# Kernel tuning notes

Hardware: AMD Instinct MI355X
Metric: run time of the kernel (lower is better)

## Reference

```python
import jax, jax.numpy as jnp
import numpy as np


def _layer_norm(x, g, b, eps=1e-5):
    mu = x.mean(-1, keepdims=True)
    var = ((x - mu) ** 2).mean(-1, keepdims=True)
    return (x - mu) * jax.lax.rsqrt(var + eps) * g + b


def _linear(x, w, b):
    # torch nn.Linear: y = x @ W^T + b, w has shape (out, in)
    return jnp.einsum('...i,oi->...o', x, w) + b


def setup_inputs() -> dict:
    key = jax.random.key(0)
    ks = jax.random.split(key, 12)
    B, N, C = 1, 512, 128
    s = 0.02  # weight init scale
    f32 = jnp.float32
    return {
        'X': jax.random.normal(ks[0], (B, N, N, C), f32),
        'mask': jax.random.randint(ks[1], (B, N, N, 1), 0, 2) > 0,
        # first LayerNorm
        'ln1_g': jnp.ones((C,), f32), 'ln1_b': jnp.zeros((C,), f32),
        # left edge MLP: Linear -> Sigmoid -> Linear
        'lw1': jax.random.normal(ks[2], (C, C), f32) * s, 'lb1': jnp.zeros((C,), f32),
        'lw2': jax.random.normal(ks[3], (C, C), f32) * s, 'lb2': jnp.zeros((C,), f32),
        # right edge MLP
        'rw1': jax.random.normal(ks[4], (C, C), f32) * s, 'rb1': jnp.zeros((C,), f32),
        'rw2': jax.random.normal(ks[5], (C, C), f32) * s, 'rb2': jnp.zeros((C,), f32),
        # skip gate: Linear -> Sigmoid
        'sw': jax.random.normal(ks[6], (C, C), f32) * s, 'sb': jnp.zeros((C,), f32),
        # combine: LayerNorm -> Linear
        'ln2_g': jnp.ones((C,), f32), 'ln2_b': jnp.zeros((C,), f32),
        'cw': jax.random.normal(ks[7], (C, C), f32) * s, 'cb': jnp.zeros((C,), f32),
    }


def reference(X, mask, ln1_g, ln1_b, lw1, lb1, lw2, lb2,
              rw1, rb1, rw2, rb2, sw, sb, ln2_g, ln2_b, cw, cb):
    h = _layer_norm(X, ln1_g, ln1_b)                      # (B,N,N,C)
    A = _linear(jax.nn.sigmoid(_linear(h, lw1, lb1)), lw2, lb2)
    Bm = _linear(jax.nn.sigmoid(_linear(h, rw1, rb1)), rw2, rb2)
    G = jax.nn.sigmoid(_linear(h, sw, sb))
    A = jnp.where(mask, A, 0.0)
    Bm = jnp.where(mask, Bm, 0.0)
    # triangle multiplication, 'outgoing': contract over k per channel
    T = jnp.einsum('bikc,bjkc->bijc', A, Bm)              # (B,N,N,C)
    Y = _linear(_layer_norm(T, ln2_g, ln2_b), cw, cb) * G
    return Y
```

## Files before the change

kernel.cpp:

```cpp
#include <hip/hip_runtime.h>

typedef unsigned short u16;
typedef unsigned int   u32;
typedef u32   u32x4  __attribute__((ext_vector_type(4)));
typedef __bf16 bf16x8 __attribute__((ext_vector_type(8)));
typedef float f32x4  __attribute__((ext_vector_type(4)));

#define NPOS (512*512)
#define WSLOT 16384

__device__ __forceinline__ u16 f2bf(float f){
  __bf16 h=(__bf16)f;
  return __builtin_bit_cast(u16,h);
}
__device__ __forceinline__ float bf2f(u16 s){ u32 u=((u32)s)<<16; return __builtin_bit_cast(float,u); }
union pk8 { u16 s[8]; u32x4 v; };

__device__ __forceinline__ void gload16(const void* g, void* l){
  __builtin_amdgcn_global_load_lds((const __attribute__((address_space(1))) void*)g,
                                   (__attribute__((address_space(3))) void*)l, 16, 0, 0);
}

__device__ __forceinline__ bf16x8 cvt8(const float* p){
  f32x4 w0=*(const f32x4*)p, w1=*(const f32x4*)(p+4);
  bf16x8 b;
#pragma unroll
  for(int e=0;e<4;e++){ b[e]=(__bf16)w0[e]; b[4+e]=(__bf16)w1[e]; }
  return b;
}

__global__ __launch_bounds__(256) void k0(
    const float* __restrict__ lw1, const float* __restrict__ lw2,
    const float* __restrict__ rw1, const float* __restrict__ rw2,
    const float* __restrict__ sw,  const float* __restrict__ cw, u16* __restrict__ Wp)
{
  const float* srcs[6]={lw1,lw2,rw1,rw2,sw,cw};
  const float* W=srcs[blockIdx.x];
  u16* dst=Wp + (size_t)blockIdx.x*WSLOT;
  const int t=threadIdx.x, lane=t&63, wvv=t>>6, lr=lane&15, quad=lane>>4;
#pragma unroll
  for(int i=0;i<8;i++){
    int tile=wvv*8+i, nt=tile>>2, kk=tile&3;
    const float* p=W+(size_t)(nt*16+lr)*128+kk*32+quad*8;
    bf16x8 b=cvt8(p);
    *(u32x4*)(dst+((size_t)tile*64+lane)*8)=__builtin_bit_cast(u32x4,b);
  }
}

__device__ __forceinline__ void wave_gemm2(const u16 (*sh)[136], int wv, int lane,
    const u16* __restrict__ Wp, const float* __restrict__ bias, float o[4][2][4])
{
  const int lr=lane&15, quad=lane>>4;
  bf16x8 b[2][4];
#pragma unroll
  for(int n2=0;n2<2;n2++){
    const int nt=wv*2+n2;
#pragma unroll
    for(int kk=0;kk<4;kk++)
      b[n2][kk]=*(const bf16x8*)(Wp+((size_t)((nt*4+kk)*64+lane))*8);
  }
  float bv[2]={bias[(wv*2)*16+lr], bias[(wv*2+1)*16+lr]};
#pragma unroll
  for(int mt=0;mt<4;mt++){
    bf16x8 a[4];
#pragma unroll
    for(int kk=0;kk<4;kk++) a[kk]=*(const bf16x8*)&sh[mt*16+lr][kk*32+quad*8];
#pragma unroll
    for(int n2=0;n2<2;n2++){
      f32x4 acc={0.f,0.f,0.f,0.f};
#pragma unroll
      for(int kk=0;kk<4;kk++)
        acc=__builtin_amdgcn_mfma_f32_16x16x32_bf16(a[kk],b[n2][kk],acc,0,0,0);
#pragma unroll
      for(int r=0;r<4;r++) o[mt][n2][r]=acc[r]+bv[n2];
    }
  }
}

__device__ __forceinline__ void sig_to_lds2(u16 (*sh)[136], int wv,int lane, float o[4][2][4]){
  const int lr=lane&15, quad=lane>>4;
#pragma unroll
  for(int mt=0;mt<4;mt++)
#pragma unroll
    for(int n2=0;n2<2;n2++)
#pragma unroll
      for(int r=0;r<4;r++)
        sh[mt*16+quad*4+r][(wv*2+n2)*16+lr]=f2bf(1.f/(1.f+__expf(-o[mt][n2][r])));
}

__device__ __forceinline__ void out_to_lds2(u16 (*sh)[136], int wv,int lane, float o[4][2][4]){
  const int lr=lane&15, quad=lane>>4;
#pragma unroll
  for(int mt=0;mt<4;mt++)
#pragma unroll
    for(int n2=0;n2<2;n2++)
#pragma unroll
      for(int r=0;r<4;r++)
        sh[mt*16+quad*4+r][(wv*2+n2)*16+lr]=f2bf(o[mt][n2][r]);
}

__device__ __forceinline__ void store_tr_m(const u16 (*sh)[136], int t, u16* __restrict__ dst,
                                           int p0, const u16* __restrict__ smask){
#pragma unroll
  for(int iter=0;iter<4;iter++){
    int c=iter*32+(t>>3);
    int pos=(t&7)*8;
    pk8 u;
#pragma unroll
    for(int r=0;r<8;r++){
      int rp=(r+(t>>3)+(t&7))&7;
      u.s[rp]=sh[pos+rp][c] & smask[pos+rp];
    }
    *(u32x4*)(dst+(size_t)c*NPOS+p0+pos)=u.v;
  }
}

__global__ __launch_bounds__(256,4) void k1(
    const float* __restrict__ X, const void* __restrict__ mask,
    const float* __restrict__ g1, const float* __restrict__ b1,
    const u16* __restrict__ Wp,
    const float* __restrict__ lb1, const float* __restrict__ lb2,
    const float* __restrict__ rb1, const float* __restrict__ rb2,
    const float* __restrict__ sb,
    u16* __restrict__ At, u16* __restrict__ Bt, float* __restrict__ G)
{
  __shared__ u16 shh[64][136];
  __shared__ u16 sht[64][136];
  __shared__ u16 smask16[64];
  __shared__ int mpacked;
  const int t=threadIdx.x;
  const int p0=blockIdx.x*64;
  if(t==0){
    const int* m32=(const int*)mask;
    int pk=0;
#pragma unroll
    for(int i=0;i<32;i++){ u32 v=(u32)m32[i]; if(v>1u) pk=1; }
    mpacked=pk;
  }
  {
    int row=t>>2, q=t&3;
    const float* xp = X + (size_t)(p0+row)*128 + q*32;
    float v[32]; float s=0.f,s2=0.f;
#pragma unroll
    for(int u=0;u<8;u++){ f32x4 d=*(const f32x4*)(xp+u*4);
#pragma unroll
      for(int e=0;e<4;e++) v[u*4+e]=d[e]; }
#pragma unroll
    for(int i=0;i<32;i++){ s+=v[i]; s2+=v[i]*v[i]; }
    s+=__shfl_xor(s,1); s2+=__shfl_xor(s2,1);
    s+=__shfl_xor(s,2); s2+=__shfl_xor(s2,2);
    float mu=s*(1.f/128.f);
    float rstd=1.f/sqrtf(s2*(1.f/128.f)-mu*mu+1e-5f);
#pragma unroll
    for(int u=0;u<4;u++){
      pk8 o;
#pragma unroll
      for(int e=0;e<8;e++){
        int c=q*32+u*8+e;
        o.s[e]=f2bf((v[u*8+e]-mu)*rstd*g1[c]+b1[c]);
      }
      *(u32x4*)&shh[row][q*32+u*8]=o.v;
    }
  }
  __syncthreads();
  if(t<64){
    int p=p0+t;
    int mval = mpacked ? (int)((const unsigned char*)mask)[p] : ((const int*)mask)[p];
    smask16[t]=(mval!=0)?(u16)0xFFFFu:(u16)0u;
  }
  const int lane=t&63, wv=t>>6, lr=lane&15, quad=lane>>4;
  float oL[4][2][4], oR[4][2][4];
  {
    float oG[4][2][4];
    wave_gemm2(shh,wv,lane,Wp+4*WSLOT,sb,oG);
#pragma unroll
    for(int mt=0;mt<4;mt++)
#pragma unroll
      for(int n2=0;n2<2;n2++)
#pragma unroll
        for(int r=0;r<4;r++){
          size_t p=p0+mt*16+quad*4+r;
          G[p*128+(wv*2+n2)*16+lr]=1.f/(1.f+__expf(-oG[mt][n2][r]));
        }
  }
  wave_gemm2(shh,wv,lane,Wp+0*WSLOT,lb1,oL);
  sig_to_lds2(sht,wv,lane,oL);
  wave_gemm2(shh,wv,lane,Wp+2*WSLOT,rb1,oR);
  __syncthreads();
  sig_to_lds2(shh,wv,lane,oR);
  wave_gemm2(sht,wv,lane,Wp+1*WSLOT,lb2,oL);
  __syncthreads();
  out_to_lds2(sht,wv,lane,oL);
  wave_gemm2(shh,wv,lane,Wp+3*WSLOT,rb2,oR);
  __syncthreads();
  store_tr_m(sht,t,At,p0,smask16);
  out_to_lds2(shh,wv,lane,oR);
  __syncthreads();
  store_tr_m(shh,t,Bt,p0,smask16);
}

__global__ __launch_bounds__(256) void k2(const u16* __restrict__ At, const u16* __restrict__ Bt,
                                          u16* __restrict__ T, int j_base, int jc, int nxsh)
{
  __shared__ u16 sA[128*64];
  __shared__ u16 sB[128*64];
  const int t=threadIdx.x, lane=t&63, wv=t>>6;
  const int bid=blockIdx.x;
  const int tpcsh=2+nxsh;
  const int xcd=bid&7, q=bid>>3;
  const int c   = xcd*16 + (q>>tpcsh);
  const int tile= q & ((1<<tpcsh)-1);
  const int j0l = (tile & ((1<<nxsh)-1))*128;
  const int i0  = (tile >> nxsh)*128;
  const int wm=(wv>>1)*64, wn=(wv&1)*64, lr=lane&15, quad=lane>>4;
  const u16* Ab = At + (size_t)c*NPOS + (size_t)i0*512;
  const u16* Bb = Bt + (size_t)c*NPOS + (size_t)(j_base+j0l)*512;
  const int srow = lane>>3;
  const int scol = ((lane&7) ^ srow)*8;
  const int swz  = (lr&7)<<4;
  f32x4 acc[4][4];
#pragma unroll
  for(int i=0;i<4;i++)
#pragma unroll
    for(int j=0;j<4;j++) acc[i][j]=(f32x4){0.f,0.f,0.f,0.f};
  for(int k0=0;k0<512;k0+=64){
#pragma unroll
    for(int j=0;j<4;j++){
      int seg=wv*4+j;
      int row=seg*8+srow;
      gload16(Ab + (size_t)row*512 + k0 + scol, &sA[seg*512]);
      gload16(Bb + (size_t)row*512 + k0 + scol, &sB[seg*512]);
    }
    __syncthreads();
    const char* sAc=(const char*)sA;
    const char* sBc=(const char*)sB;
#pragma unroll
    for(int ks=0;ks<2;ks++){
      bf16x8 a[4],b[4];
#pragma unroll
      for(int mt=0;mt<4;mt++){
        int row=wm+mt*16+lr;
        a[mt]=*(const bf16x8*)(sAc + row*128 + ((ks*64+quad*16)^swz));
      }
#pragma unroll
      for(int nt=0;nt<4;nt++){
        int row=wn+nt*16+lr;
        b[nt]=*(const bf16x8*)(sBc + row*128 + ((ks*64+quad*16)^swz));
      }
#pragma unroll
      for(int mt=0;mt<4;mt++)
#pragma unroll
        for(int nt=0;nt<4;nt++)
          acc[mt][nt]=__builtin_amdgcn_mfma_f32_16x16x32_bf16(a[mt],b[nt],acc[mt][nt],0,0,0);
    }
    __syncthreads();
  }
  u16* Tb = T + (size_t)c*512*jc;
#pragma unroll
  for(int mt=0;mt<4;mt++)
#pragma unroll
    for(int nt=0;nt<4;nt++)
#pragma unroll
      for(int r=0;r<4;r++){
        int row=i0+wm+mt*16+quad*4+r;
        int col=j0l+wn+nt*16+lr;
        Tb[(size_t)row*jc+col]=f2bf(acc[mt][nt][r]);
      }
}

__global__ __launch_bounds__(256) void k3(const u16* __restrict__ T,
    const u16* __restrict__ cwp,
    const float* __restrict__ g2, const float* __restrict__ b2,
    const float* __restrict__ cb, float* GY,
    int j_base, int jc, int jshift)
{
  __shared__ u16 sH[128][136];
  const int t=threadIdx.x;
  const int cp0=blockIdx.x*128;
  {
    int c=t>>1, half=t&1;
    const u16* Tp = T + (size_t)c*512*jc + cp0 + half*64;
#pragma unroll
    for(int u=0;u<8;u++){
      pk8 d; d.v=*(const u32x4*)(Tp+u*8);
#pragma unroll
      for(int e=0;e<8;e++) sH[half*64+u*8+e][c]=d.s[e];
    }
  }
  __syncthreads();
  {
    int pos=t>>1, half=t&1;
    float v[64]; float s=0.f,s2=0.f;
#pragma unroll
    for(int u=0;u<8;u++)
#pragma unroll
      for(int e=0;e<8;e++){ float x=bf2f(sH[pos][half*64+u*8+e]); v[u*8+e]=x; s+=x; s2+=x*x; }
    s+=__shfl_xor(s,1); s2+=__shfl_xor(s2,1);
    float mu=s*(1.f/128.f);
    float rstd=1.f/sqrtf(s2*(1.f/128.f)-mu*mu+1e-5f);
#pragma unroll
    for(int u=0;u<8;u++){
      pk8 o;
#pragma unroll
      for(int e=0;e<8;e++){
        int c=half*64+u*8+e;
        o.s[e]=f2bf((v[u*8+e]-mu)*rstd*g2[c]+b2[c]);
      }
      *(u32x4*)&sH[pos][half*64+u*8]=o.v;
    }
  }
  __syncthreads();
  const int lane=t&63, wv=t>>6, m0=wv*32, lr=lane&15, quad=lane>>4;
  bf16x8 a[2][4];
#pragma unroll
  for(int mt=0;mt<2;mt++)
#pragma unroll
    for(int kk=0;kk<4;kk++) a[mt][kk]=*(const bf16x8*)&sH[m0+mt*16+lr][kk*32+quad*8];
#pragma unroll
  for(int nt=0;nt<8;nt++){
    f32x4 a0={0.f,0.f,0.f,0.f}, a1={0.f,0.f,0.f,0.f};
#pragma unroll
    for(int kk=0;kk<4;kk++){
      bf16x8 b=*(const bf16x8*)(cwp+((size_t)((nt*4+kk)*64+lane))*8);
      a0=__builtin_amdgcn_mfma_f32_16x16x32_bf16(a[0][kk],b,a0,0,0,0);
      a1=__builtin_amdgcn_mfma_f32_16x16x32_bf16(a[1][kk],b,a1,0,0,0);
    }
    float cbv=cb[nt*16+lr];
#pragma unroll
    for(int mt=0;mt<2;mt++){
      f32x4 ac = mt? a1: a0;
#pragma unroll
      for(int r=0;r<4;r++){
        int l=m0+mt*16+quad*4+r;
        int pl=cp0+l;
        size_t p=((size_t)(pl>>jshift)<<9)+(size_t)j_base+(pl&(jc-1));
        int col=nt*16+lr;
        float gg=GY[p*128+col];
        GY[p*128+col]=(ac[r]+cbv)*gg;
      }
    }
  }
}

__global__ void kprobe(float* out, u32 wsmib){
  if(threadIdx.x==0 && blockIdx.x==0) out[0]=(float)wsmib;
}

extern "C" void kernel_launch(void* const* d_in, const int* in_sizes, int n_in,
                              void* d_out, int out_size, void* d_ws, size_t ws_size,
                              hipStream_t stream)
{
  (void)in_sizes; (void)n_in; (void)out_size;
  const float* X  =(const float*)d_in[0];
  const void*  mask=d_in[1];
  const float* g1 =(const float*)d_in[2];  const float* b1 =(const float*)d_in[3];
  const float* lw1=(const float*)d_in[4];  const float* lb1=(const float*)d_in[5];
  const float* lw2=(const float*)d_in[6];  const float* lb2=(const float*)d_in[7];
  const float* rw1=(const float*)d_in[8];  const float* rb1=(const float*)d_in[9];
  const float* rw2=(const float*)d_in[10]; const float* rb2=(const float*)d_in[11];
  const float* sw =(const float*)d_in[12]; const float* sb =(const float*)d_in[13];
  const float* g2 =(const float*)d_in[14]; const float* b2 =(const float*)d_in[15];
  const float* cw =(const float*)d_in[16]; const float* cb =(const float*)d_in[17];
  float* out=(float*)d_out;

  const size_t wbytes = (size_t)6*WSLOT*sizeof(u16);
  const size_t base = wbytes + 2*(size_t)NPOS*128*sizeof(u16);
  int jc=0, jshift=0, nxsh=0;
  if      (ws_size >= base + (size_t)512*512*128*2){ jc=512; jshift=9; nxsh=2; }
  else if (ws_size >= base + (size_t)512*256*128*2){ jc=256; jshift=8; nxsh=1; }
  else if (ws_size >= base + (size_t)512*128*128*2){ jc=128; jshift=7; nxsh=0; }
  if(jc==0){
    kprobe<<<dim3(1),dim3(64),0,stream>>>(out,(u32)(ws_size>>20));
    return;
  }
  u16* Wp=(u16*)d_ws;
  u16* At=Wp+(size_t)6*WSLOT;
  u16* Bt=At+(size_t)NPOS*128;
  u16* T =Bt+(size_t)NPOS*128;

  k0<<<dim3(6),dim3(256),0,stream>>>(lw1,lw2,rw1,rw2,sw,cw,Wp);
  k1<<<dim3(4096),dim3(256),0,stream>>>(X,mask,g1,b1,Wp,lb1,lb2,rb1,rb2,sb,At,Bt,out);
  const int nbl=(jc/128)*4*128;
  for(int jb=0;jb<512;jb+=jc){
    k2<<<dim3(nbl),dim3(256),0,stream>>>(At,Bt,T,jb,jc,nxsh);
    k3<<<dim3(4*jc),dim3(256),0,stream>>>(T,Wp+(size_t)5*WSLOT,g2,b2,cb,out,jb,jc,jshift);
  }
}
```

Before: 555.0 us.

## Store gate in bf16, double-buffer k2 LDS loads, reorder k1 for register pressure

The sigmoid gate G is now kept as bf16 in workspace instead of fp32 in the output buffer. This halves gate write and read traffic between k1 and k3, at some precision cost. k2 double-buffers its shared-memory A/B tiles so the next k-step's global-to-LDS loads overlap the current MFMAs. k1 processes the left, right and gate paths one after another with a single LDS scratch buffer and applies the mask as a float multiply, to cut live registers. k3 also re-reads LDS instead of holding 64 floats per thread. Together these add more barriers in k1 and double k2's LDS footprint.

```diff
diff --git a/kernel.cpp b/kernel.cpp
--- a/kernel.cpp
+++ b/kernel.cpp
@@ -88,19 +88,20 @@
         sh[mt*16+quad*4+r][(wv*2+n2)*16+lr]=f2bf(1.f/(1.f+__expf(-o[mt][n2][r])));
 }
 
-__device__ __forceinline__ void out_to_lds2(u16 (*sh)[136], int wv,int lane, float o[4][2][4]){
+__device__ __forceinline__ void mask_to_lds2(u16 (*sh)[136], int wv,int lane, float o[4][2][4], const float* smask){
   const int lr=lane&15, quad=lane>>4;
 #pragma unroll
   for(int mt=0;mt<4;mt++)
 #pragma unroll
     for(int n2=0;n2<2;n2++)
 #pragma unroll
-      for(int r=0;r<4;r++)
-        sh[mt*16+quad*4+r][(wv*2+n2)*16+lr]=f2bf(o[mt][n2][r]);
-}
-
-__device__ __forceinline__ void store_tr_m(const u16 (*sh)[136], int t, u16* __restrict__ dst,
-                                           int p0, const u16* __restrict__ smask){
+      for(int r=0;r<4;r++){
+        int row=mt*16+quad*4+r;
+        sh[row][(wv*2+n2)*16+lr]=f2bf(o[mt][n2][r]*smask[row]);
+      }
+}
+
+__device__ __forceinline__ void store_tr(const u16 (*sh)[136], int t, u16* __restrict__ dst, int p0){
 #pragma unroll
   for(int iter=0;iter<4;iter++){
     int c=iter*32+(t>>3);
@@ -109,7 +110,7 @@
 #pragma unroll
     for(int r=0;r<8;r++){
       int rp=(r+(t>>3)+(t&7))&7;
-      u.s[rp]=sh[pos+rp][c] & smask[pos+rp];
+      u.s[rp]=sh[pos+rp][c];
     }
     *(u32x4*)(dst+(size_t)c*NPOS+p0+pos)=u.v;
   }
@@ -122,11 +123,12 @@
     const float* __restrict__ lb1, const float* __restrict__ lb2,
     const float* __restrict__ rb1, const float* __restrict__ rb2,
     const float* __restrict__ sb,
-    u16* __restrict__ At, u16* __restrict__ Bt, float* __restrict__ G)
+    u16* __restrict__ At, u16* __restrict__ Bt,
+    u16* __restrict__ Gb, float* __restrict__ Gf, int gb16)
 {
   __shared__ u16 shh[64][136];
   __shared__ u16 sht[64][136];
-  __shared__ u16 smask16[64];
+  __shared__ float smask[64];
   __shared__ int mpacked;
   const int t=threadIdx.x;
   const int p0=blockIdx.x*64;
@@ -166,44 +168,47 @@
   if(t<64){
     int p=p0+t;
     int mval = mpacked ? (int)((const unsigned char*)mask)[p] : ((const int*)mask)[p];
-    smask16[t]=(mval!=0)?(u16)0xFFFFu:(u16)0u;
-  }
-  const int lane=t&63, wv=t>>6, lr=lane&15, quad=lane>>4;
+    smask[t]=(mval!=0)?1.f:0.f;
+  }
+  const int lane=t&63, wv=t>>6;
   float oL[4][2][4], oR[4][2][4];
-  {
-    float oG[4][2][4];
-    wave_gemm2(shh,wv,lane,Wp+4*WSLOT,sb,oG);
-#pragma unroll
-    for(int mt=0;mt<4;mt++)
-#pragma unroll
-      for(int n2=0;n2<2;n2++)
-#pragma unroll
-        for(int r=0;r<4;r++){
-          size_t p=p0+mt*16+quad*4+r;
-          G[p*128+(wv*2+n2)*16+lr]=1.f/(1.f+__expf(-oG[mt][n2][r]));
-        }
-  }
   wave_gemm2(shh,wv,lane,Wp+0*WSLOT,lb1,oL);
   sig_to_lds2(sht,wv,lane,oL);
+  __syncthreads();
+  wave_gemm2(sht,wv,lane,Wp+1*WSLOT,lb2,oL);
+  __syncthreads();
+  mask_to_lds2(sht,wv,lane,oL,smask);
+  __syncthreads();
+  store_tr(sht,t,At,p0);
   wave_gemm2(shh,wv,lane,Wp+2*WSLOT,rb1,oR);
   __syncthreads();
-  sig_to_lds2(shh,wv,lane,oR);
-  wave_gemm2(sht,wv,lane,Wp+1*WSLOT,lb2,oL);
-  __syncthreads();
-  out_to_lds2(sht,wv,lane,oL);
-  wave_gemm2(shh,wv,lane,Wp+3*WSLOT,rb2,oR);
-  __syncthreads();
-  store_tr_m(sht,t,At,p0,smask16);
-  out_to_lds2(shh,wv,lane,oR);
-  __syncthreads();
-  store_tr_m(shh,t,Bt,p0,smask16);
+  sig_to_lds2(sht,wv,lane,oR);
+  __syncthreads();
+  wave_gemm2(sht,wv,lane,Wp+3*WSLOT,rb2,oR);
+  __syncthreads();
+  mask_to_lds2(sht,wv,lane,oR,smask);
+  __syncthreads();
+  store_tr(sht,t,Bt,p0);
+  wave_gemm2(shh,wv,lane,Wp+4*WSLOT,sb,oL);
+  const int lr=lane&15, quad=lane>>4;
+#pragma unroll
+  for(int mt=0;mt<4;mt++)
+#pragma unroll
+    for(int n2=0;n2<2;n2++)
+#pragma unroll
+      for(int r=0;r<4;r++){
+        size_t p=p0+mt*16+quad*4+r;
+        float sg=1.f/(1.f+__expf(-oL[mt][n2][r]));
+        size_t idx=p*128+(wv*2+n2)*16+lr;
+        if(gb16) Gb[idx]=f2bf(sg); else Gf[idx]=sg;
+      }
 }
 
 __global__ __launch_bounds__(256) void k2(const u16* __restrict__ At, const u16* __restrict__ Bt,
                                           u16* __restrict__ T, int j_base, int jc, int nxsh)
 {
-  __shared__ u16 sA[128*64];
-  __shared__ u16 sB[128*64];
+  __shared__ u16 sA[2][8192];
+  __shared__ u16 sB[2][8192];
   const int t=threadIdx.x, lane=t&63, wv=t>>6;
   const int bid=blockIdx.x;
   const int tpcsh=2+nxsh;
@@ -218,22 +223,29 @@
   const int srow = lane>>3;
   const int scol = ((lane&7) ^ srow)*8;
   const int swz  = (lr&7)<<4;
+
   f32x4 acc[4][4];
 #pragma unroll
   for(int i=0;i<4;i++)
 #pragma unroll
     for(int j=0;j<4;j++) acc[i][j]=(f32x4){0.f,0.f,0.f,0.f};
-  for(int k0=0;k0<512;k0+=64){
-#pragma unroll
-    for(int j=0;j<4;j++){
-      int seg=wv*4+j;
-      int row=seg*8+srow;
-      gload16(Ab + (size_t)row*512 + k0 + scol, &sA[seg*512]);
-      gload16(Bb + (size_t)row*512 + k0 + scol, &sB[seg*512]);
-    }
-    __syncthreads();
-    const char* sAc=(const char*)sA;
-    const char* sBc=(const char*)sB;
+
+#define K2_STAGE(buf,k0) {                                              \
+    _Pragma("unroll")                                                   \
+    for(int j=0;j<4;j++){                                               \
+      int seg=wv*4+j;                                                   \
+      int row=seg*8+srow;                                               \
+      gload16(Ab + (size_t)row*512 + (k0) + scol, &sA[buf][seg*512]);   \
+      gload16(Bb + (size_t)row*512 + (k0) + scol, &sB[buf][seg*512]);   \
+    } }
+
+  K2_STAGE(0,0)
+  __syncthreads();
+  int cur=0;
+  for(int it=0; it<8; ++it){
+    if(it<7) K2_STAGE(cur^1,(it+1)*64)
+    const char* sAc=(const char*)sA[cur];
+    const char* sBc=(const char*)sB[cur];
 #pragma unroll
     for(int ks=0;ks<2;ks++){
       bf16x8 a[4],b[4];
@@ -254,7 +266,9 @@
           acc[mt][nt]=__builtin_amdgcn_mfma_f32_16x16x32_bf16(a[mt],b[nt],acc[mt][nt],0,0,0);
     }
     __syncthreads();
-  }
+    cur^=1;
+  }
+#undef K2_STAGE
   u16* Tb = T + (size_t)c*512*jc;
 #pragma unroll
   for(int mt=0;mt<4;mt++)
@@ -271,8 +285,9 @@
 __global__ __launch_bounds__(256) void k3(const u16* __restrict__ T,
     const u16* __restrict__ cwp,
     const float* __restrict__ g2, const float* __restrict__ b2,
-    const float* __restrict__ cb, float* GY,
-    int j_base, int jc, int jshift)
+    const float* __restrict__ cb,
+    const u16* __restrict__ Gb, float* GY,
+    int j_base, int jc, int jshift, int gb16)
 {
   __shared__ u16 sH[128][136];
   const int t=threadIdx.x;
@@ -290,21 +305,24 @@
   __syncthreads();
   {
     int pos=t>>1, half=t&1;
-    float v[64]; float s=0.f,s2=0.f;
-#pragma unroll
-    for(int u=0;u<8;u++)
-#pragma unroll
-      for(int e=0;e<8;e++){ float x=bf2f(sH[pos][half*64+u*8+e]); v[u*8+e]=x; s+=x; s2+=x*x; }
+    float s=0.f,s2=0.f;
+#pragma unroll
+    for(int u=0;u<8;u++){
+      pk8 d; d.v=*(const u32x4*)&sH[pos][half*64+u*8];
+#pragma unroll
+      for(int e=0;e<8;e++){ float x=bf2f(d.s[e]); s+=x; s2+=x*x; }
+    }
     s+=__shfl_xor(s,1); s2+=__shfl_xor(s2,1);
     float mu=s*(1.f/128.f);
     float rstd=1.f/sqrtf(s2*(1.f/128.f)-mu*mu+1e-5f);
 #pragma unroll
     for(int u=0;u<8;u++){
+      pk8 d; d.v=*(const u32x4*)&sH[pos][half*64+u*8];
       pk8 o;
 #pragma unroll
       for(int e=0;e<8;e++){
         int c=half*64+u*8+e;
-        o.s[e]=f2bf((v[u*8+e]-mu)*rstd*g2[c]+b2[c]);
+        o.s[e]=f2bf((bf2f(d.s[e])-mu)*rstd*g2[c]+b2[c]);
       }
       *(u32x4*)&sH[pos][half*64+u*8]=o.v;
     }
@@ -335,8 +353,13 @@
         int pl=cp0+l;
         size_t p=((size_t)(pl>>jshift)<<9)+(size_t)j_base+(pl&(jc-1));
         int col=nt*16+lr;
-        float gg=GY[p*128+col];
-        GY[p*128+col]=(ac[r]+cbv)*gg;
+        size_t idx=p*128+col;
+        if(gb16){
+          GY[idx]=(ac[r]+cbv)*bf2f(Gb[idx]);
+        }else{
+          float gg=GY[idx];
+          GY[idx]=(ac[r]+cbv)*gg;
+        }
       }
     }
   }
@@ -364,11 +387,16 @@
   float* out=(float*)d_out;
 
   const size_t wbytes = (size_t)6*WSLOT*sizeof(u16);
-  const size_t base = wbytes + 2*(size_t)NPOS*128*sizeof(u16);
-  int jc=0, jshift=0, nxsh=0;
-  if      (ws_size >= base + (size_t)512*512*128*2){ jc=512; jshift=9; nxsh=2; }
-  else if (ws_size >= base + (size_t)512*256*128*2){ jc=256; jshift=8; nxsh=1; }
-  else if (ws_size >= base + (size_t)512*128*128*2){ jc=128; jshift=7; nxsh=0; }
+  const size_t szAB   = 2*(size_t)NPOS*128*sizeof(u16);
+  const size_t szG    = (size_t)NPOS*128*sizeof(u16);
+  const size_t base   = wbytes + szAB;
+  int jc=0, jshift=0, nxsh=0, gb=0;
+  if      (ws_size >= base + (size_t)512*512*128*2 + szG){ jc=512; jshift=9; nxsh=2; gb=1; }
+  else if (ws_size >= base + (size_t)512*512*128*2)      { jc=512; jshift=9; nxsh=2; gb=0; }
+  else if (ws_size >= base + (size_t)512*256*128*2 + szG){ jc=256; jshift=8; nxsh=1; gb=1; }
+  else if (ws_size >= base + (size_t)512*256*128*2)      { jc=256; jshift=8; nxsh=1; gb=0; }
+  else if (ws_size >= base + (size_t)512*128*128*2 + szG){ jc=128; jshift=7; nxsh=0; gb=1; }
+  else if (ws_size >= base + (size_t)512*128*128*2)      { jc=128; jshift=7; nxsh=0; gb=0; }
   if(jc==0){
     kprobe<<<dim3(1),dim3(64),0,stream>>>(out,(u32)(ws_size>>20));
     return;
@@ -377,12 +405,13 @@
   u16* At=Wp+(size_t)6*WSLOT;
   u16* Bt=At+(size_t)NPOS*128;
   u16* T =Bt+(size_t)NPOS*128;
+  u16* Gb=T +(size_t)512*jc*128;
 
   k0<<<dim3(6),dim3(256),0,stream>>>(lw1,lw2,rw1,rw2,sw,cw,Wp);
-  k1<<<dim3(4096),dim3(256),0,stream>>>(X,mask,g1,b1,Wp,lb1,lb2,rb1,rb2,sb,At,Bt,out);
+  k1<<<dim3(4096),dim3(256),0,stream>>>(X,mask,g1,b1,Wp,lb1,lb2,rb1,rb2,sb,At,Bt,Gb,out,gb);
   const int nbl=(jc/128)*4*128;
   for(int jb=0;jb<512;jb+=jc){
     k2<<<dim3(nbl),dim3(256),0,stream>>>(At,Bt,T,jb,jc,nxsh);
-    k3<<<dim3(4*jc),dim3(256),0,stream>>>(T,Wp+(size_t)5*WSLOT,g2,b2,cb,out,jb,jc,jshift);
-  }
-}
+    k3<<<dim3(4*jc),dim3(256),0,stream>>>(T,Wp+(size_t)5*WSLOT,g2,b2,cb,Gb,out,jb,jc,jshift,gb);
+  }
+}
```

After: 570.2 us. 2.7% more time.
